# Kernel optimization log

Hardware: AMD Instinct MI355X
Metric: run time of the kernel (lower is better)

The kernel has to match this reference:

```python
import jax, jax.numpy as jnp
import numpy as np
import math

B, S, D, DFF, E, K = 8, 2048, 1024, 4096, 8, 2
CAP_FACTOR = 1.6   # n_experts=8 > 6 branch in __init__
NOISE_STD = 0.02   # n_experts=8 > 6 branch in __init__


def setup_inputs() -> dict:
    key = jax.random.key(0)
    ks = jax.random.split(key, 6)
    x = jax.random.normal(ks[0], (B, S, D), jnp.float32)
    noise = jax.random.normal(ks[1], (B * S, E), jnp.float32)  # router exploration noise
    router_w = jax.random.normal(ks[2], (E, D), jnp.float32) * 0.02
    router_b = jnp.zeros((E,), jnp.float32)
    w1 = jax.random.normal(ks[3], (E, D, DFF), jnp.float32) * 0.02
    b1 = jnp.zeros((E, DFF), jnp.float32)
    w2 = jax.random.normal(ks[4], (E, DFF, D), jnp.float32) * 0.02
    b2 = jnp.zeros((E, D), jnp.float32)
    return {"x": x, "noise": noise, "router_w": router_w, "router_b": router_b,
            "w1": w1, "b1": b1, "w2": w2, "b2": b2}


def reference(x, noise, router_w, router_b, w1, b1, w2, b2):
    b, s, d = x.shape
    T = b * s
    x_flat = x.reshape(T, d)
    # Router: logits + gaussian exploration noise (randn_like * noise_std)
    logits = x_flat @ router_w.T + router_b + noise * NOISE_STD
    probs = jax.nn.softmax(logits, axis=-1)
    _, topk_idx = jax.lax.top_k(probs, K)  # [T, K]
    capacity = math.ceil(T * CAP_FACTOR / E)  # static
    # Pad row T: gathers of dropped slots read zeros; scatters to it are discarded.
    x_pad = jnp.concatenate([x_flat, jnp.zeros((1, d), x_flat.dtype)], axis=0)
    out = jnp.zeros((T + 1, d), x_flat.dtype)
    # NOTE: original writes (not weighted-adds) expert outputs; later experts
    # overwrite earlier ones for tokens routed to both. Loop order matters.
    for i in range(E):
        mask = (topk_idx == i).any(axis=-1)  # [T]
        # first `capacity` tokens in order (matches token_indices[:capacity]);
        # padded slots get index T.
        idx = jnp.nonzero(mask, size=capacity, fill_value=T)[0]
        inp = x_pad[idx]                                   # [cap, d]
        h = jax.nn.gelu(inp @ w1[i] + b1[i], approximate=False)
        eo = h @ w2[i] + b2[i]                             # [cap, d]
        out = out.at[idx].set(eo)
    return out[:T].reshape(b, s, d)
```

## Files before the change

### kernel.cpp

```cpp
#include <hip/hip_runtime.h>
#include <math.h>

#define T_TOK   16384
#define DMODEL  1024
#define DFF     4096
#define NEXP    8
#define CAPACITY 3277
#define CAP_PAD  3328

typedef unsigned short u16;
typedef __attribute__((ext_vector_type(8))) __bf16 bf16x8;
typedef __attribute__((ext_vector_type(4))) float  f32x4;

#define W1T_OFF   0ull
#define W2T_OFF   67108864ull
#define XG_OFF    134217728ull
#define H_OFF     171966464ull
#define TOPK_OFF  322961408ull
#define CCNT_OFF  323092480ull
#define CBASE_OFF 323096576ull
#define LISTS_OFF 323100672ull
#define CNT_OFF   323207168ull
#define OFFS_OFF  323207200ull
#define PCNT_OFF  323207296ull

__device__ __forceinline__ u16 f2bf(float x) {
  union { float f; unsigned u; } v; v.f = x;
  unsigned r = v.u + 0x7fffu + ((v.u >> 16) & 1u);
  return (u16)(r >> 16);
}

__device__ __forceinline__ void async_cp16(const void* g, void* l) {
  __builtin_amdgcn_global_load_lds((const __attribute__((address_space(1))) void*)g,
                                   (__attribute__((address_space(3))) void*)l,
                                   16, 0, 0);
}

__device__ __forceinline__ void barrier_fence() {
  asm volatile("" ::: "memory");
  __builtin_amdgcn_s_barrier();
  asm volatile("" ::: "memory");
}

__global__ __launch_bounds__(256) void transpose_cvt64(const float* __restrict__ src,
                                                       u16* __restrict__ dst, int R, int C) {
  int tilesC = C >> 6;
  int per_e = (R >> 6) * tilesC;
  int bid = blockIdx.x;
  int e = bid / per_e, rem = bid % per_e;
  int rt = rem / tilesC, ct = rem % tilesC;
  const float* s = src + (size_t)e * R * C;
  u16* d = dst + (size_t)e * R * C;
  __shared__ u16 tile[64][70];
  int tid = threadIdx.x;
  int rr = tid >> 4;
  int c4 = (tid & 15) << 2;
#pragma unroll
  for (int i = 0; i < 4; ++i) {
    int r = rr + i * 16;
    float4 v = *(const float4*)(s + (size_t)(rt*64 + r) * C + ct*64 + c4);
    tile[r][c4+0] = f2bf(v.x);
    tile[r][c4+1] = f2bf(v.y);
    tile[r][c4+2] = f2bf(v.z);
    tile[r][c4+3] = f2bf(v.w);
  }
  __syncthreads();
#pragma unroll
  for (int k = 0; k < 2; ++k) {
    int idx = k*256 + tid;
    int c  = idx >> 3;
    int rc = (idx & 7) << 3;
    union { u16 u[8]; uint4 v; } pk;
#pragma unroll
    for (int j = 0; j < 8; ++j) pk.u[j] = tile[rc + j][c];
    *(uint4*)(d + (size_t)(ct*64 + c) * R + rt*64 + rc) = pk.v;
  }
}

__global__ __launch_bounds__(256) void router_topk(const float* __restrict__ x,
    const float* __restrict__ rw, const float* __restrict__ rb,
    const float* __restrict__ noise, int* __restrict__ topk) {
  int w = threadIdx.x >> 6, lane = threadIdx.x & 63;
  int t = blockIdx.x * 4 + w;
  const float* xr = x + (size_t)t * DMODEL;
  double acc[NEXP];
#pragma unroll
  for (int e = 0; e < NEXP; ++e) acc[e] = 0.0;
  for (int c = lane; c < DMODEL; c += 64) {
    float xv = xr[c];
#pragma unroll
    for (int e = 0; e < NEXP; ++e) acc[e] += (double)xv * (double)rw[e*DMODEL + c];
  }
#pragma unroll
  for (int e = 0; e < NEXP; ++e) {
#pragma unroll
    for (int off = 32; off > 0; off >>= 1) acc[e] += __shfl_down(acc[e], off, 64);
  }
  if (lane == 0) {
    double best = -1e300, sec = -1e300; int bi = 0, si = 0;
#pragma unroll
    for (int e = 0; e < NEXP; ++e) {
      double v = acc[e] + (double)rb[e] + (double)noise[(size_t)t*NEXP + e] * 0.02;
      if (v > best)     { sec = best; si = bi; best = v; bi = e; }
      else if (v > sec) { sec = v; si = e; }
    }
    topk[2*t] = bi; topk[2*t+1] = si;
  }
}

__global__ __launch_bounds__(128) void chunk_count(const int* __restrict__ topk,
                                                   int* __restrict__ ccnt) {
  int tid = threadIdx.x, lane = tid & 63, w = tid >> 6;
  int t = blockIdx.x*128 + tid;
  int i0 = topk[2*t], i1 = topk[2*t+1];
  __shared__ int cnt[2][NEXP];
#pragma unroll
  for (int e = 0; e < NEXP; ++e) {
    unsigned long long bal = __ballot((i0 == e) || (i1 == e));
    if (lane == 0) cnt[w][e] = __popcll(bal);
  }
  __syncthreads();
  if (tid < NEXP) ccnt[blockIdx.x*NEXP + tid] = cnt[0][tid] + cnt[1][tid];
}

__global__ void chunk_prefix(const int* __restrict__ ccnt, int* __restrict__ cbase) {
  int e = threadIdx.x;
  if (e < NEXP) {
    int run = 0;
    for (int c = 0; c < 128; ++c) { cbase[c*NEXP + e] = run; run += ccnt[c*NEXP + e]; }
  }
}

__global__ __launch_bounds__(128) void assign_compact(const int* __restrict__ topk,
    const int* __restrict__ cbase, int* __restrict__ counts, int* __restrict__ lists) {
  int chunk = blockIdx.x, tid = threadIdx.x;
  int lane = tid & 63, w = tid >> 6;
  int t = chunk*128 + tid;
  int i0 = topk[2*t], i1 = topk[2*t+1];
  __shared__ int w0cnt[NEXP];
  unsigned long long below = (1ull << lane) - 1ull;
#pragma unroll
  for (int e = 0; e < NEXP; ++e) {
    unsigned long long bal = __ballot((i0 == e) || (i1 == e));
    if (w == 0 && lane == 0) w0cnt[e] = __popcll(bal);
  }
  __syncthreads();
  int fin = -1;
#pragma unroll
  for (int e = 0; e < NEXP; ++e) {
    bool m = (i0 == e) || (i1 == e);
    unsigned long long bal = __ballot(m);
    int rank = cbase[chunk*NEXP + e] + (w ? w0cnt[e] : 0) + __popcll(bal & below);
    if (m && rank < CAPACITY) fin = e;
  }
#pragma unroll
  for (int e = 0; e < NEXP; ++e) {
    bool m = (fin == e);
    unsigned long long bal = __ballot(m);
    int c = __popcll(bal);
    if (c) {
      int leader = __ffsll((unsigned long long)bal) - 1;
      int base = 0;
      if (lane == leader) base = atomicAdd(&counts[e], c);
      base = __shfl(base, leader, 64);
      if (m) lists[e*CAP_PAD + base + __popcll(bal & below)] = t;
    }
  }
}

__global__ void calc_offsets(const int* __restrict__ counts, int* __restrict__ offs,
                             int* __restrict__ pcnt) {
  if (threadIdx.x == 0) {
    int run = 0;
    for (int e = 0; e < NEXP; ++e) {
      offs[e] = run;
      int pc = ((counts[e] + 255) >> 8) << 8;
      pcnt[e] = pc;
      run += pc;
    }
    offs[NEXP] = run;
  }
}

__global__ __launch_bounds__(128) void gather_x(const float* __restrict__ x,
    const int* __restrict__ lists, const int* __restrict__ counts,
    const int* __restrict__ offs, const int* __restrict__ pcnt, u16* __restrict__ xg) {
  int bid = blockIdx.x;
  int e = bid / CAP_PAD, r = bid % CAP_PAD;
  if (r >= pcnt[e]) return;
  unsigned long long* dst = (unsigned long long*)(xg + (size_t)(offs[e] + r) * DMODEL);
  int tid = threadIdx.x;
  if (r < counts[e]) {
    const float4* src = (const float4*)(x + (size_t)lists[e*CAP_PAD + r] * DMODEL);
#pragma unroll
    for (int i = 0; i < 2; ++i) {
      float4 v = src[tid + i*128];
      unsigned long long pk = (unsigned long long)f2bf(v.x)
                            | ((unsigned long long)f2bf(v.y) << 16)
                            | ((unsigned long long)f2bf(v.z) << 32)
                            | ((unsigned long long)f2bf(v.w) << 48);
      dst[tid + i*128] = pk;
    }
  } else {
#pragma unroll
    for (int i = 0; i < 2; ++i) dst[tid + i*128] = 0ull;
  }
}


template<int S>
__device__ __forceinline__ void stage_half(const u16* __restrict__ g, int row0, int k0,
                                           u16* tile, int half, int tid) {
  int wid  = tid >> 6;
  int rloc = tid >> 3;
  int cb   = (tid & 7) << 4;
  int scb  = cb ^ ((rloc & 7) << 4);
#pragma unroll
  for (int j = 0; j < 2; ++j) {
    int r = half*128 + j*64 + rloc;
    const u16* src = g + (size_t)(row0 + r) * S + k0 + (scb >> 1);
    u16* dst = tile + half*8192 + j*4096 + wid*512;
    async_cp16(src, dst);
  }
}

__device__ __forceinline__ bf16x8 ldsfrag(const u16* tile, int r, int cb) {
  int a = r*128 + (cb ^ ((r & 7) << 4));
  return *(const bf16x8*)((const char*)tile + a);
}

template<int KELEM, int NTOT, int EPI>
__global__ __launch_bounds__(512, 2) void ffn_gemm8(
    const u16* __restrict__ Abase, const u16* __restrict__ Btall,
    const float* __restrict__ bias,
    const int* __restrict__ offs, const int* __restrict__ pcnt,
    const int* __restrict__ counts, const int* __restrict__ lists,
    u16* __restrict__ Hout, float* __restrict__ Fout) {
  constexpr int NKT = KELEM / 64;
  int e = blockIdx.z, mt = blockIdx.y, nt = blockIdx.x;
  int pc = pcnt[e];
  int m0 = mt * 256;
  if (m0 >= pc) return;
  int n0 = nt * 256;
  int tid = threadIdx.x, lane = tid & 63, wid = tid >> 6;
  int wm = wid >> 2, wn = wid & 3;
  const u16* A = Abase + (size_t)offs[e] * KELEM;
  const u16* B = Btall + (size_t)e * NTOT * KELEM;
  __shared__ __align__(16) u16 lds[2][2][16384];

  stage_half<KELEM>(A, m0, 0,  (u16*)lds[0][0], 0, tid);
  stage_half<KELEM>(A, m0, 0,  (u16*)lds[0][0], 1, tid);
  stage_half<KELEM>(B, n0, 0,  (u16*)lds[0][1], 0, tid);
  stage_half<KELEM>(B, n0, 0,  (u16*)lds[0][1], 1, tid);
  stage_half<KELEM>(B, n0, 64, (u16*)lds[1][1], 0, tid);
  stage_half<KELEM>(B, n0, 64, (u16*)lds[1][1], 1, tid);
  asm volatile("s_waitcnt vmcnt(4)" ::: "memory");
  barrier_fence();

  int frow = lane & 15;
  int fk   = (lane >> 4) << 4;
  f32x4 acc[8][4] = {};

#pragma unroll 2
  for (int t = 0; t < NKT; ++t) {
    int cur = t & 1;
    u16* As_ = (u16*)lds[cur][0];
    u16* Bs_ = (u16*)lds[cur][1];
    u16* An_ = (u16*)lds[cur ^ 1][0];
    bf16x8 a[4][2], bb[2][2][2];

#pragma unroll
    for (int f = 0; f < 4; ++f)
#pragma unroll
      for (int kk = 0; kk < 2; ++kk)
        a[f][kk] = ldsfrag(As_, wm*128 + f*16 + frow, kk*64 + fk);
#pragma unroll
    for (int f = 0; f < 2; ++f)
#pragma unroll
      for (int kk = 0; kk < 2; ++kk)
        bb[0][f][kk] = ldsfrag(Bs_, wn*64 + f*16 + frow, kk*64 + fk);
    if (t + 1 < NKT) stage_half<KELEM>(A, m0, (t+1)*64, An_, 0, tid);
    barrier_fence();
    __builtin_amdgcn_s_setprio(1);
#pragma unroll
    for (int f = 0; f < 4; ++f)
#pragma unroll
      for (int g = 0; g < 2; ++g)
#pragma unroll
        for (int kk = 0; kk < 2; ++kk)
          acc[f][g] = __builtin_amdgcn_mfma_f32_16x16x32_bf16(a[f][kk], bb[0][g][kk], acc[f][g], 0, 0, 0);
    __builtin_amdgcn_s_setprio(0);
    barrier_fence();

#pragma unroll
    for (int f = 0; f < 2; ++f)
#pragma unroll
      for (int kk = 0; kk < 2; ++kk)
        bb[1][f][kk] = ldsfrag(Bs_, wn*64 + (2+f)*16 + frow, kk*64 + fk);
    if (t + 1 < NKT) stage_half<KELEM>(A, m0, (t+1)*64, An_, 1, tid);
    barrier_fence();
    __builtin_amdgcn_s_setprio(1);
#pragma unroll
    for (int f = 0; f < 4; ++f)
#pragma unroll
      for (int g = 0; g < 2; ++g)
#pragma unroll
        for (int kk = 0; kk < 2; ++kk)
          acc[f][2+g] = __builtin_amdgcn_mfma_f32_16x16x32_bf16(a[f][kk], bb[1][g][kk], acc[f][2+g], 0, 0, 0);
    __builtin_amdgcn_s_setprio(0);
    barrier_fence();

#pragma unroll
    for (int f = 0; f < 4; ++f)
#pragma unroll
      for (int kk = 0; kk < 2; ++kk)
        a[f][kk] = ldsfrag(As_, wm*128 + 64 + f*16 + frow, kk*64 + fk);
    if (t + 2 < NKT) stage_half<KELEM>(B, n0, (t+2)*64, Bs_, 0, tid);
    barrier_fence();
    __builtin_amdgcn_s_setprio(1);
#pragma unroll
    for (int f = 0; f < 4; ++f)
#pragma unroll
      for (int g = 0; g < 2; ++g)
#pragma unroll
        for (int kk = 0; kk < 2; ++kk)
          acc[4+f][g] = __builtin_amdgcn_mfma_f32_16x16x32_bf16(a[f][kk], bb[0][g][kk], acc[4+f][g], 0, 0, 0);
    __builtin_amdgcn_s_setprio(0);
    barrier_fence();

    if (t + 2 < NKT) stage_half<KELEM>(B, n0, (t+2)*64, Bs_, 1, tid);
    barrier_fence();
    __builtin_amdgcn_s_setprio(1);
#pragma unroll
    for (int f = 0; f < 4; ++f)
#pragma unroll
      for (int g = 0; g < 2; ++g)
#pragma unroll
        for (int kk = 0; kk < 2; ++kk)
          acc[4+f][2+g] = __builtin_amdgcn_mfma_f32_16x16x32_bf16(a[f][kk], bb[1][g][kk], acc[4+f][2+g], 0, 0, 0);
    __builtin_amdgcn_s_setprio(0);
    if (t + 2 < NKT)      asm volatile("s_waitcnt vmcnt(4)" ::: "memory");
    else if (t + 1 < NKT) asm volatile("s_waitcnt vmcnt(0)" ::: "memory");
    barrier_fence();
  }

  if constexpr (EPI == 0) {
    const float* be = bias + e * NTOT;
    u16* H = Hout + (size_t)offs[e] * NTOT;
    u16* mybuf = ((u16*)lds) + wid * 1280;
    float bv[4];
#pragma unroll
    for (int g = 0; g < 4; ++g) bv[g] = be[n0 + wn*64 + g*16 + frow];
    int r4 = (lane >> 4) * 4;
#pragma unroll
    for (int f = 0; f < 8; ++f) {
#pragma unroll
      for (int g = 0; g < 4; ++g)
#pragma unroll
        for (int r = 0; r < 4; ++r) {
          float v = acc[f][g][r] + bv[g];
          float gl = 0.5f * v * (1.0f + erff(v * 0.70710678118654752f));
          mybuf[(r4 + r) * 72 + g*16 + frow] = f2bf(gl);
        }
      asm volatile("s_waitcnt lgkmcnt(0)" ::: "memory");
#pragma unroll
      for (int rr = 0; rr < 2; ++rr) {
        int row = (lane >> 3) + rr*8;
        int cb  = lane & 7;
        bf16x8 vv = *(const bf16x8*)(mybuf + row*72 + cb*8);
        *(bf16x8*)(H + (size_t)(m0 + wm*128 + f*16 + row) * NTOT + n0 + wn*64 + cb*8) = vv;
      }
      asm volatile("s_waitcnt lgkmcnt(0)" ::: "memory");
    }
  } else {
    int cnt = counts[e];
    const float* be = bias + e * NTOT;
    const int* le = lists + e * CAP_PAD;
    float* mybuf = (float*)((u16*)lds + wid * 2304);
    float bv[4];
#pragma unroll
    for (int g = 0; g < 4; ++g) bv[g] = be[n0 + wn*64 + g*16 + frow];
    int r4 = (lane >> 4) * 4;
#pragma unroll
    for (int f = 0; f < 8; ++f) {
#pragma unroll
      for (int g = 0; g < 4; ++g)
#pragma unroll
        for (int r = 0; r < 4; ++r)
          mybuf[(r4 + r) * 68 + g*16 + frow] = acc[f][g][r] + bv[g];
      asm volatile("s_waitcnt lgkmcnt(0)" ::: "memory");
      int row = lane >> 2, cg = lane & 3;
      int grow = m0 + wm*128 + f*16 + row;
      if (grow < cnt) {
        int tk = le[grow];
        float* po = Fout + (size_t)tk * DMODEL + n0 + wn*64 + cg*16;
        const float* pb = mybuf + row*68 + cg*16;
#pragma unroll
        for (int j = 0; j < 4; ++j)
          *(f32x4*)(po + j*4) = *(const f32x4*)(pb + j*4);
      }
      asm volatile("s_waitcnt lgkmcnt(0)" ::: "memory");
    }
  }
}

extern "C" void kernel_launch(void* const* d_in, const int* in_sizes, int n_in,
                              void* d_out, int out_size, void* d_ws, size_t ws_size,
                              hipStream_t stream) {
  const float* x     = (const float*)d_in[0];
  const float* noise = (const float*)d_in[1];
  const float* rw    = (const float*)d_in[2];
  const float* rb    = (const float*)d_in[3];
  const float* w1    = (const float*)d_in[4];
  const float* b1    = (const float*)d_in[5];
  const float* w2    = (const float*)d_in[6];
  const float* b2    = (const float*)d_in[7];
  float* out = (float*)d_out;
  char* ws = (char*)d_ws;

  u16* w1t   = (u16*)(ws + W1T_OFF);
  u16* w2t   = (u16*)(ws + W2T_OFF);
  u16* xg    = (u16*)(ws + XG_OFF);
  u16* hbuf  = (u16*)(ws + H_OFF);
  int* topk  = (int*)(ws + TOPK_OFF);
  int* ccnt  = (int*)(ws + CCNT_OFF);
  int* cbase = (int*)(ws + CBASE_OFF);
  int* lists = (int*)(ws + LISTS_OFF);
  int* cnts  = (int*)(ws + CNT_OFF);
  int* offs  = (int*)(ws + OFFS_OFF);
  int* pcnt  = (int*)(ws + PCNT_OFF);

  hipMemsetAsync(d_out, 0, (size_t)T_TOK * DMODEL * sizeof(float), stream);
  hipMemsetAsync(cnts, 0, NEXP * sizeof(int), stream);

  transpose_cvt64<<<NEXP*(DMODEL/64)*(DFF/64), 256, 0, stream>>>(w1, w1t, DMODEL, DFF);
  transpose_cvt64<<<NEXP*(DFF/64)*(DMODEL/64), 256, 0, stream>>>(w2, w2t, DFF, DMODEL);
  router_topk<<<T_TOK/4, 256, 0, stream>>>(x, rw, rb, noise, topk);
  chunk_count<<<128, 128, 0, stream>>>(topk, ccnt);
  chunk_prefix<<<1, 64, 0, stream>>>(ccnt, cbase);
  assign_compact<<<128, 128, 0, stream>>>(topk, cbase, cnts, lists);
  calc_offsets<<<1, 64, 0, stream>>>(cnts, offs, pcnt);
  gather_x<<<NEXP*CAP_PAD, 128, 0, stream>>>(x, lists, cnts, offs, pcnt, xg);
  ffn_gemm8<DMODEL, DFF, 0><<<dim3(DFF/256, CAP_PAD/256, NEXP), 512, 0, stream>>>(
      xg, w1t, b1, offs, pcnt, cnts, lists, hbuf, nullptr);
  ffn_gemm8<DFF, DMODEL, 1><<<dim3(DMODEL/256, CAP_PAD/256, NEXP), 512, 0, stream>>>(
      hbuf, w2t, b2, offs, pcnt, cnts, lists, nullptr, out);
}
```

Measured before the change: 745.9 us.

## Zero only dropped output rows, grid-stride gather, swizzled epilogue staging

Replaces the full 64 MB memset of the output with a kernel that zeroes only the rows of tokens that no expert accepted, using a per-token accept flag written in assign_compact. gather_x becomes a grid-stride loop over a fixed 4096 blocks instead of one block per row. The GEMM1 epilogue stages the whole 128x64 bf16 warp tile in XOR-swizzled LDS and writes it out in one pass rather than per 16-row chunk with extra waits. The transpose also packs bf16 pairs into 32-bit LDS stores. The risks are extra LDS use in the epilogue and correctness that depends on every accepted row being fully written by GEMM2.

```diff
diff --git a/kernel.cpp b/kernel.cpp
--- a/kernel.cpp
+++ b/kernel.cpp
@@ -23,6 +23,7 @@
 #define CNT_OFF   323207168ull
 #define OFFS_OFF  323207200ull
 #define PCNT_OFF  323207296ull
+#define ACC_OFF   323207424ull
 
 __device__ __forceinline__ u16 f2bf(float x) {
   union { float f; unsigned u; } v; v.f = x;
@@ -59,10 +60,10 @@
   for (int i = 0; i < 4; ++i) {
     int r = rr + i * 16;
     float4 v = *(const float4*)(s + (size_t)(rt*64 + r) * C + ct*64 + c4);
-    tile[r][c4+0] = f2bf(v.x);
-    tile[r][c4+1] = f2bf(v.y);
-    tile[r][c4+2] = f2bf(v.z);
-    tile[r][c4+3] = f2bf(v.w);
+    unsigned lo = (unsigned)f2bf(v.x) | ((unsigned)f2bf(v.y) << 16);
+    unsigned hi = (unsigned)f2bf(v.z) | ((unsigned)f2bf(v.w) << 16);
+    *(unsigned*)&tile[r][c4]     = lo;
+    *(unsigned*)&tile[r][c4 + 2] = hi;
   }
   __syncthreads();
 #pragma unroll
@@ -132,7 +133,8 @@
 }
 
 __global__ __launch_bounds__(128) void assign_compact(const int* __restrict__ topk,
-    const int* __restrict__ cbase, int* __restrict__ counts, int* __restrict__ lists) {
+    const int* __restrict__ cbase, int* __restrict__ counts, int* __restrict__ lists,
+    int* __restrict__ accept) {
   int chunk = blockIdx.x, tid = threadIdx.x;
   int lane = tid & 63, w = tid >> 6;
   int t = chunk*128 + tid;
@@ -153,6 +155,7 @@
     int rank = cbase[chunk*NEXP + e] + (w ? w0cnt[e] : 0) + __popcll(bal & below);
     if (m && rank < CAPACITY) fin = e;
   }
+  accept[t] = (fin >= 0) ? 1 : 0;
 #pragma unroll
   for (int e = 0; e < NEXP; ++e) {
     bool m = (fin == e);
@@ -182,28 +185,42 @@
   }
 }
 
+__global__ __launch_bounds__(256) void zero_dropped(const int* __restrict__ accept,
+                                                    float* __restrict__ out) {
+  int lane = threadIdx.x & 63, w = threadIdx.x >> 6;
+  for (int tok = blockIdx.x*4 + w; tok < T_TOK; tok += gridDim.x*4) {
+    if (!accept[tok]) {
+      float4 z = make_float4(0.f, 0.f, 0.f, 0.f);
+      float4* p = (float4*)(out + (size_t)tok * DMODEL);
+#pragma unroll
+      for (int i = 0; i < 4; ++i) p[lane + i*64] = z;
+    }
+  }
+}
+
 __global__ __launch_bounds__(128) void gather_x(const float* __restrict__ x,
     const int* __restrict__ lists, const int* __restrict__ counts,
     const int* __restrict__ offs, const int* __restrict__ pcnt, u16* __restrict__ xg) {
-  int bid = blockIdx.x;
-  int e = bid / CAP_PAD, r = bid % CAP_PAD;
-  if (r >= pcnt[e]) return;
-  unsigned long long* dst = (unsigned long long*)(xg + (size_t)(offs[e] + r) * DMODEL);
   int tid = threadIdx.x;
-  if (r < counts[e]) {
-    const float4* src = (const float4*)(x + (size_t)lists[e*CAP_PAD + r] * DMODEL);
-#pragma unroll
-    for (int i = 0; i < 2; ++i) {
-      float4 v = src[tid + i*128];
-      unsigned long long pk = (unsigned long long)f2bf(v.x)
-                            | ((unsigned long long)f2bf(v.y) << 16)
-                            | ((unsigned long long)f2bf(v.z) << 32)
-                            | ((unsigned long long)f2bf(v.w) << 48);
-      dst[tid + i*128] = pk;
-    }
-  } else {
-#pragma unroll
-    for (int i = 0; i < 2; ++i) dst[tid + i*128] = 0ull;
+  for (int idx = blockIdx.x; idx < NEXP*CAP_PAD; idx += gridDim.x) {
+    int e = idx / CAP_PAD, r = idx % CAP_PAD;
+    if (r >= pcnt[e]) continue;
+    unsigned long long* dst = (unsigned long long*)(xg + (size_t)(offs[e] + r) * DMODEL);
+    if (r < counts[e]) {
+      const float4* src = (const float4*)(x + (size_t)lists[e*CAP_PAD + r] * DMODEL);
+#pragma unroll
+      for (int i = 0; i < 2; ++i) {
+        float4 v = src[tid + i*128];
+        unsigned long long pk = (unsigned long long)f2bf(v.x)
+                              | ((unsigned long long)f2bf(v.y) << 16)
+                              | ((unsigned long long)f2bf(v.z) << 32)
+                              | ((unsigned long long)f2bf(v.w) << 48);
+        dst[tid + i*128] = pk;
+      }
+    } else {
+#pragma unroll
+      for (int i = 0; i < 2; ++i) dst[tid + i*128] = 0ull;
+    }
   }
 }
 
@@ -347,31 +364,33 @@
   if constexpr (EPI == 0) {
     const float* be = bias + e * NTOT;
     u16* H = Hout + (size_t)offs[e] * NTOT;
-    u16* mybuf = ((u16*)lds) + wid * 1280;
+    char* mybuf = (char*)lds + wid * 16384;
     float bv[4];
 #pragma unroll
     for (int g = 0; g < 4; ++g) bv[g] = be[n0 + wn*64 + g*16 + frow];
     int r4 = (lane >> 4) * 4;
 #pragma unroll
-    for (int f = 0; f < 8; ++f) {
+    for (int f = 0; f < 8; ++f)
 #pragma unroll
       for (int g = 0; g < 4; ++g)
 #pragma unroll
         for (int r = 0; r < 4; ++r) {
           float v = acc[f][g][r] + bv[g];
           float gl = 0.5f * v * (1.0f + erff(v * 0.70710678118654752f));
-          mybuf[(r4 + r) * 72 + g*16 + frow] = f2bf(gl);
+          int rr = f*16 + r4 + r;
+          int cb = (g*16 + frow) * 2;
+          *(u16*)(mybuf + rr*128 + (cb ^ ((rr & 7) << 4))) = f2bf(gl);
         }
-      asm volatile("s_waitcnt lgkmcnt(0)" ::: "memory");
-#pragma unroll
-      for (int rr = 0; rr < 2; ++rr) {
-        int row = (lane >> 3) + rr*8;
-        int cb  = lane & 7;
-        bf16x8 vv = *(const bf16x8*)(mybuf + row*72 + cb*8);
-        *(bf16x8*)(H + (size_t)(m0 + wm*128 + f*16 + row) * NTOT + n0 + wn*64 + cb*8) = vv;
+    asm volatile("s_waitcnt lgkmcnt(0)" ::: "memory");
+#pragma unroll
+    for (int rb = 0; rb < 8; ++rb)
+#pragma unroll
+      for (int kk = 0; kk < 2; ++kk) {
+        int rr = rb*16 + frow;
+        int c8 = kk*4 + (lane >> 4);
+        bf16x8 vv = *(const bf16x8*)(mybuf + rr*128 + ((c8*16) ^ ((rr & 7) << 4)));
+        *(bf16x8*)(H + (size_t)(m0 + wm*128 + rr) * NTOT + n0 + wn*64 + c8*8) = vv;
       }
-      asm volatile("s_waitcnt lgkmcnt(0)" ::: "memory");
-    }
   } else {
     int cnt = counts[e];
     const float* be = bias + e * NTOT;
@@ -429,8 +448,8 @@
   int* cnts  = (int*)(ws + CNT_OFF);
   int* offs  = (int*)(ws + OFFS_OFF);
   int* pcnt  = (int*)(ws + PCNT_OFF);
-
-  hipMemsetAsync(d_out, 0, (size_t)T_TOK * DMODEL * sizeof(float), stream);
+  int* accfl = (int*)(ws + ACC_OFF);
+
   hipMemsetAsync(cnts, 0, NEXP * sizeof(int), stream);
 
   transpose_cvt64<<<NEXP*(DMODEL/64)*(DFF/64), 256, 0, stream>>>(w1, w1t, DMODEL, DFF);
@@ -438,9 +457,10 @@
   router_topk<<<T_TOK/4, 256, 0, stream>>>(x, rw, rb, noise, topk);
   chunk_count<<<128, 128, 0, stream>>>(topk, ccnt);
   chunk_prefix<<<1, 64, 0, stream>>>(ccnt, cbase);
-  assign_compact<<<128, 128, 0, stream>>>(topk, cbase, cnts, lists);
+  assign_compact<<<128, 128, 0, stream>>>(topk, cbase, cnts, lists, accfl);
   calc_offsets<<<1, 64, 0, stream>>>(cnts, offs, pcnt);
-  gather_x<<<NEXP*CAP_PAD, 128, 0, stream>>>(x, lists, cnts, offs, pcnt, xg);
+  zero_dropped<<<512, 256, 0, stream>>>(accfl, out);
+  gather_x<<<4096, 128, 0, stream>>>(x, lists, cnts, offs, pcnt, xg);
   ffn_gemm8<DMODEL, DFF, 0><<<dim3(DFF/256, CAP_PAD/256, NEXP), 512, 0, stream>>>(
       xg, w1t, b1, offs, pcnt, cnts, lists, hbuf, nullptr);
   ffn_gemm8<DFF, DMODEL, 1><<<dim3(DMODEL/256, CAP_PAD/256, NEXP), 512, 0, stream>>>(
```

Result: faster. 726.4 us (-2.6%).
